# Kernel optimization log

Measured on AMD Instinct MI355X. Metric: run time of the kernel, lower is better.

The kernel has to match this reference:

```python
import jax, jax.numpy as jnp
import numpy as np

B, C, H, W = 2, 64, 64, 64
N = H * W

def _leaky(x):
    return jnp.where(x > 0, x, 0.1 * x)

def _conv1x1(x, w, b):
    # x: (B,C,H,W), w: (O,C), b: (O,)
    return jnp.einsum('bchw,oc->bohw', x, w) + b[None, :, None, None]

def _conv3x3(x, w, b=None):
    y = jax.lax.conv_general_dilated(x, w, (1, 1), 'SAME',
                                     dimension_numbers=('NCHW', 'OIHW', 'NCHW'))
    if b is not None:
        y = y + b[None, :, None, None]
    return y

def _add_coords(x):
    b, c, h, w = x.shape
    xx = (jnp.arange(w, dtype=x.dtype) / (w - 1)) * 2 - 1  # varies along width (last axis)
    yy = (jnp.arange(h, dtype=x.dtype) / (h - 1)) * 2 - 1  # varies along height
    xx = jnp.broadcast_to(xx[None, None, None, :], (b, 1, h, w))
    yy = jnp.broadcast_to(yy[None, None, :, None], (b, 1, h, w))
    return jnp.concatenate([x, xx, yy], axis=1)

def _channel_attn(x, lw, lb):
    # AdaptiveAvgPool2d(1) -> Linear(1,1) -> LeakyReLU(0.1) -> same Linear(1,1) -> Sigmoid
    p = x.mean(axis=(2, 3), keepdims=True)  # (B,C,1,1)
    h = _leaky(p * lw + lb)
    return jax.nn.sigmoid(h * lw + lb)

def _gated(x, lw, lb, coord_w):
    return _channel_attn(x, lw, lb) * _conv3x3(_add_coords(x), coord_w)

def reference(x, guide, lin_w, lin_b, coord_w,
              xq_w, xq_b, xk_w, xk_b, xv_w, xv_b,
              gq_w, gq_b, gk_w, gk_b,
              gamma, alpha, c1_w, c1_b, c2_w, c2_b, sc_w, sc_b):
    b, c, h, w = x.shape
    n = h * w
    xg = _gated(x, lin_w, lin_b, coord_w)       # (B,C,H,W)
    gg = _gated(guide, lin_w, lin_b, coord_w)

    xq = _conv1x1(xg, xq_w, xq_b).reshape(b, c, n)
    xk = _conv1x1(xg, xk_w, xk_b).reshape(b, c, n)
    xv = _conv1x1(xg, xv_w, xv_b).reshape(b, c, n)
    x_attn = jax.nn.softmax(jnp.einsum('bcn,bcm->bnm', xq, xk), axis=-1)  # (B,N,N)
    x_out = jnp.einsum('bcm,bnm->bcn', xv, x_attn).reshape(b, c, h, w)

    gq = _conv1x1(gg, gq_w, gq_b).reshape(b, c, n)
    gk = _conv1x1(gg, gk_w, gk_b).reshape(b, c, n)
    g_attn = jax.nn.softmax(jnp.einsum('bcn,bcm->bnm', gq, gk), axis=-1)  # (B,N,N)
    # guide_out deliberately uses x_value (as in the original forward)
    guide_out = jnp.einsum('bcm,bnm->bcn', xv, g_attn).reshape(b, c, h, w)

    out = gamma * x_out + alpha * guide_out
    branch = _conv3x3(_leaky(_conv3x3(_leaky(out), c1_w, c1_b)), c2_w, c2_b)
    return branch + _conv1x1(out, sc_w, sc_b) * guide_out

def setup_inputs() -> dict:
    key = jax.random.key(0)
    ks = jax.random.split(key, 32)
    f32 = jnp.float32
    def w1(k, o, i):
        return jax.random.normal(k, (o, i), f32) / np.sqrt(i).astype(np.float32)
    def w3(k, o, i):
        return jax.random.normal(k, (o, i, 3, 3), f32) / np.sqrt(i * 9).astype(np.float32)
    def bv(k, o):
        return jax.random.normal(k, (o,), f32) * 0.01
    return {
        'x': jax.random.normal(ks[0], (B, C, H, W), f32),
        'guide': jax.random.normal(ks[1], (B, C, H, W), f32),
        'lin_w': jax.random.normal(ks[2], (), f32),
        'lin_b': jax.random.normal(ks[3], (), f32) * 0.01,
        'coord_w': w3(ks[4], C, C + 2),
        'xq_w': w1(ks[5], C, C), 'xq_b': bv(ks[6], C),
        'xk_w': w1(ks[7], C, C), 'xk_b': bv(ks[8], C),
        'xv_w': w1(ks[9], C, C), 'xv_b': bv(ks[10], C),
        'gq_w': w1(ks[11], C, C), 'gq_b': bv(ks[12], C),
        'gk_w': w1(ks[13], C, C), 'gk_b': bv(ks[14], C),
        'gamma': jax.random.normal(ks[15], (1,), f32) * 0.5,
        'alpha': jax.random.normal(ks[16], (1,), f32) * 0.5,
        'c1_w': w3(ks[17], C, C), 'c1_b': bv(ks[18], C),
        'c2_w': w3(ks[19], C, C), 'c2_b': bv(ks[20], C),
        'sc_w': w1(ks[21], C, C), 'sc_b': bv(ks[22], C),
    }
```

## Files before the change

### kernel.cpp

```cpp
#include <hip/hip_runtime.h>
#include <hip/hip_bf16.h>

using bf16 = __hip_bfloat16;

#define DI __device__ __forceinline__

typedef __attribute__((ext_vector_type(8))) short short8;
typedef __attribute__((ext_vector_type(8))) unsigned short u16x8;
typedef __attribute__((ext_vector_type(4))) unsigned short u16x4;
typedef __attribute__((ext_vector_type(4))) float f32x4;

#define MFMA_BF16 __builtin_amdgcn_mfma_f32_16x16x32_bf16

DI float leaky(float x) { return x > 0.f ? x : 0.1f * x; }

DI unsigned short b16(float x) {
  union { float f; unsigned u; } v; v.f = x;
  unsigned r = v.u + 0x7FFFu + ((v.u >> 16) & 1u);
  return (unsigned short)(r >> 16);
}
DI float fromb16(unsigned short h) {
  union { unsigned u; float f; } v; v.u = ((unsigned)h) << 16; return v.f;
}

static constexpr int N_ = 4096;
static constexpr size_t CN = 262144;
static constexpr size_t BCN = 524288;

static constexpr size_t XG_OFF = 137104;
static constexpr size_t GG_OFF = XG_OFF + BCN;
static constexpr size_t QX_OFF = GG_OFF + BCN;
static constexpr size_t KX_OFF = QX_OFF + BCN;
static constexpr size_t VX_OFF = KX_OFF + BCN;
static constexpr size_t QG_OFF = VX_OFF + BCN;
static constexpr size_t KG_OFF = QG_OFF + BCN;
static constexpr size_t P1X_OFF = KG_OFF + BCN;
static constexpr size_t P1G_OFF = P1X_OFF + BCN;
static constexpr size_t ML_OFF  = P1G_OFF + BCN;
static constexpr size_t MLL_OFF = ML_OFF + 32768;
static constexpr size_t CA_OFF = ML_OFF;
static constexpr size_t OB_OFF = QX_OFF;
static constexpr size_t UB_OFF = KX_OFF;
static constexpr size_t GO_OFF = GG_OFF;
static constexpr size_t QXH_U = QX_OFF * 2, QXL_U = QXH_U + BCN;
static constexpr size_t KXH_U = KX_OFF * 2, KXL_U = KXH_U + BCN;
static constexpr size_t VXH_U = VX_OFF * 2;
static constexpr size_t QGH_U = QG_OFF * 2, QGL_U = QGH_U + BCN;
static constexpr size_t KGH_U = KG_OFF * 2, KGL_U = KGH_U + BCN;

__global__ __launch_bounds__(64) void k_ca(const float* __restrict__ x,
                                           const float* __restrict__ g,
                                           const float* __restrict__ lw_p,
                                           const float* __restrict__ lb_p,
                                           float* __restrict__ ws) {
  int blk = blockIdx.x;
  int ch = blk & 63; blk >>= 6;
  int b  = blk & 1;  blk >>= 1;
  int src = blk;
  const float* in = (src ? g : x) + ((size_t)(b * 64 + ch)) * N_;
  int t = threadIdx.x;
  float s = 0.f;
#pragma unroll
  for (int i = 0; i < 16; ++i) {
    float4 v = *reinterpret_cast<const float4*>(in + i * 256 + t * 4);
    s += (v.x + v.y) + (v.z + v.w);
  }
#pragma unroll
  for (int d = 1; d < 64; d <<= 1) s += __shfl_xor(s, d, 64);
  if (t == 0) {
    float p = s * (1.f / 4096.f);
    float lwv = lw_p[0], lbv = lb_p[0];
    float h = leaky(lwv * p + lbv);
    ws[CA_OFF + (src * 2 + b) * 64 + ch] = 1.f / (1.f + expf(-(lwv * h + lbv)));
  }
}

__global__ __launch_bounds__(256) void k_coordconv(const float* __restrict__ x,
                                                   const float* __restrict__ g,
                                                   const float* __restrict__ cw,
                                                   float* __restrict__ ws) {
  int blk = blockIdx.x;
  int row = blk & 63; blk >>= 6;
  int og  = blk & 15; blk >>= 4;
  int b   = blk & 1;  blk >>= 1;
  int src = blk;
  int o0 = og * 4;
  const float* in = src ? g : x;
  float* outp = ws + (src ? GG_OFF : XG_OFF);
  __shared__ __align__(16) float4 wl4[594];
  __shared__ float part[4][4][64];
  int t = threadIdx.x;
  int wv = t >> 6, px = t & 63;
  {
    float* wlf = (float*)wl4;
    for (int idx = t; idx < 2376; idx += 256)
      wlf[idx] = cw[(size_t)(o0 + (idx & 3)) * 594 + (idx >> 2)];
  }
  int rm = row - 1, rp = row + 1;
  int rmc = rm < 0 ? 0 : rm, rpc = rp > 63 ? 63 : rp;
  float maskm = rm < 0 ? 0.f : 1.f, maskp = rp > 63 ? 0.f : 1.f;
  int c0 = wv * 16;
  const float* base = in + ((size_t)(b * 64 + c0)) * N_ + px;
  float ra[16], rb[16], rc[16];
#pragma unroll
  for (int i = 0; i < 16; ++i) {
    ra[i] = base[(size_t)i * N_ + (size_t)rmc * 64] * maskm;
    rb[i] = base[(size_t)i * N_ + (size_t)row * 64];
    rc[i] = base[(size_t)i * N_ + (size_t)rpc * 64] * maskp;
  }
  float acc[4] = {};
  auto tap9 = [&](int ch, float va, float vb, float vc) {
    float la = __shfl_up(va, 1, 64);   if (px == 0)  la = 0.f;
    float ga = __shfl_down(va, 1, 64); if (px == 63) ga = 0.f;
    float lb = __shfl_up(vb, 1, 64);   if (px == 0)  lb = 0.f;
    float gb = __shfl_down(vb, 1, 64); if (px == 63) gb = 0.f;
    float lc = __shfl_up(vc, 1, 64);   if (px == 0)  lc = 0.f;
    float gc = __shfl_down(vc, 1, 64); if (px == 63) gc = 0.f;
    float4 w0 = wl4[ch * 9 + 0], w1 = wl4[ch * 9 + 1], w2 = wl4[ch * 9 + 2];
    float4 w3 = wl4[ch * 9 + 3], w4 = wl4[ch * 9 + 4], w5 = wl4[ch * 9 + 5];
    float4 w6 = wl4[ch * 9 + 6], w7 = wl4[ch * 9 + 7], w8 = wl4[ch * 9 + 8];
    acc[0] = fmaf(w0.x, la, fmaf(w1.x, va, fmaf(w2.x, ga, acc[0])));
    acc[1] = fmaf(w0.y, la, fmaf(w1.y, va, fmaf(w2.y, ga, acc[1])));
    acc[2] = fmaf(w0.z, la, fmaf(w1.z, va, fmaf(w2.z, ga, acc[2])));
    acc[3] = fmaf(w0.w, la, fmaf(w1.w, va, fmaf(w2.w, ga, acc[3])));
    acc[0] = fmaf(w3.x, lb, fmaf(w4.x, vb, fmaf(w5.x, gb, acc[0])));
    acc[1] = fmaf(w3.y, lb, fmaf(w4.y, vb, fmaf(w5.y, gb, acc[1])));
    acc[2] = fmaf(w3.z, lb, fmaf(w4.z, vb, fmaf(w5.z, gb, acc[2])));
    acc[3] = fmaf(w3.w, lb, fmaf(w4.w, vb, fmaf(w5.w, gb, acc[3])));
    acc[0] = fmaf(w6.x, lc, fmaf(w7.x, vc, fmaf(w8.x, gc, acc[0])));
    acc[1] = fmaf(w6.y, lc, fmaf(w7.y, vc, fmaf(w8.y, gc, acc[1])));
    acc[2] = fmaf(w6.z, lc, fmaf(w7.z, vc, fmaf(w8.z, gc, acc[2])));
    acc[3] = fmaf(w6.w, lc, fmaf(w7.w, vc, fmaf(w8.w, gc, acc[3])));
  };
  __syncthreads();
#pragma unroll
  for (int i = 0; i < 16; ++i) tap9(c0 + i, ra[i], rb[i], rc[i]);
  if (wv == 3) {
    float xx = (float)px * (2.f / 63.f) - 1.f;
    tap9(64, maskm * xx, xx, maskp * xx);
    float ya = maskm * ((float)rm * (2.f / 63.f) - 1.f);
    float yb = (float)row * (2.f / 63.f) - 1.f;
    float yc = maskp * ((float)rp * (2.f / 63.f) - 1.f);
    tap9(65, ya, yb, yc);
  }
#pragma unroll
  for (int oo = 0; oo < 4; ++oo) part[wv][oo][px] = acc[oo];
  __syncthreads();
  int oc = t >> 6;
  float s = (part[0][oc][px] + part[1][oc][px]) + (part[2][oc][px] + part[3][oc][px]);
  float cav = ws[CA_OFF + (src * 2 + b) * 64 + o0 + oc];
  outp[((size_t)(b * 64 + o0 + oc)) * N_ + (size_t)row * 64 + px] = s * cav;
}

__global__ __launch_bounds__(256) void k_proj(float* __restrict__ ws,
                                              const float* __restrict__ xqw, const float* __restrict__ xqb,
                                              const float* __restrict__ xkw, const float* __restrict__ xkb,
                                              const float* __restrict__ xvw, const float* __restrict__ xvb,
                                              const float* __restrict__ gqw, const float* __restrict__ gqb,
                                              const float* __restrict__ gkw, const float* __restrict__ gkb) {
  int blk = blockIdx.x;
  int pt = blk & 63; blk >>= 6;
  int b  = blk & 1;  blk >>= 1;
  int which = blk;
  size_t in_o;
  const float *wp, *bp;
  size_t hU = 0, lU = 0;
  if (which == 0)      { in_o = XG_OFF; wp = xqw; bp = xqb; hU = QXH_U; lU = QXL_U; }
  else if (which == 1) { in_o = XG_OFF; wp = xkw; bp = xkb; hU = KXH_U; lU = KXL_U; }
  else if (which == 2) { in_o = XG_OFF; wp = xvw; bp = xvb; }
  else if (which == 3) { in_o = GG_OFF; wp = gqw; bp = gqb; hU = QGH_U; lU = QGL_U; }
  else                 { in_o = GG_OFF; wp = gkw; bp = gkb; hU = KGH_U; lU = KGL_U; }

  __shared__ float tile[64 * 64];
  __shared__ float wl[64 * 65];
  __shared__ float bl[64];
  unsigned short* us = (unsigned short*)ws;
  int t = threadIdx.x;
  int pb = pt * 64;
  const float* in0 = ws + in_o + (size_t)b * CN + pb;
  for (int c0 = (t >> 6); c0 < 64; c0 += 4)
    tile[c0 * 64 + (t & 63)] = in0[(size_t)c0 * N_ + (t & 63)];
  for (int idx = t; idx < 4096; idx += 256)
    wl[(idx >> 6) * 65 + (idx & 63)] = wp[idx];
  if (t < 64) bl[t] = bp[t];
  __syncthreads();
  int o = t & 63, grp = t >> 6;
  const float* wr = &wl[o * 65];
  float acc[16];
  float bv = bl[o];
#pragma unroll
  for (int j = 0; j < 16; ++j) acc[j] = bv;
  for (int c = 0; c < 64; ++c) {
    float wv = wr[c];
    const float4* tb = reinterpret_cast<const float4*>(&tile[c * 64 + grp * 16]);
    float4 t0 = tb[0], t1 = tb[1], t2 = tb[2], t3 = tb[3];
    acc[0] = fmaf(wv, t0.x, acc[0]);   acc[1] = fmaf(wv, t0.y, acc[1]);
    acc[2] = fmaf(wv, t0.z, acc[2]);   acc[3] = fmaf(wv, t0.w, acc[3]);
    acc[4] = fmaf(wv, t1.x, acc[4]);   acc[5] = fmaf(wv, t1.y, acc[5]);
    acc[6] = fmaf(wv, t1.z, acc[6]);   acc[7] = fmaf(wv, t1.w, acc[7]);
    acc[8] = fmaf(wv, t2.x, acc[8]);   acc[9] = fmaf(wv, t2.y, acc[9]);
    acc[10] = fmaf(wv, t2.z, acc[10]); acc[11] = fmaf(wv, t2.w, acc[11]);
    acc[12] = fmaf(wv, t3.x, acc[12]); acc[13] = fmaf(wv, t3.y, acc[13]);
    acc[14] = fmaf(wv, t3.z, acc[14]); acc[15] = fmaf(wv, t3.w, acc[15]);
  }
  if (which != 2) {
#pragma unroll
    for (int j = 0; j < 16; ++j) {
      size_t idx = ((size_t)b * N_ + pb + grp * 16 + j) * 64 + o;
      unsigned short hi = b16(acc[j]);
      us[hU + idx] = hi;
      us[lU + idx] = b16(acc[j] - fromb16(hi));
    }
  } else {
    __syncthreads();
    float* ot = wl;
#pragma unroll
    for (int j = 0; j < 16; ++j) ot[o * 65 + grp * 16 + j] = acc[j];
    __syncthreads();
    int o2 = t >> 2;
#pragma unroll
    for (int e = 0; e < 4; ++e) {
      int px = (t & 3) * 16 + e * 4;
      u16x4 hv;
#pragma unroll
      for (int q = 0; q < 4; ++q) hv[q] = b16(ot[o2 * 65 + px + q]);
      size_t idx = ((size_t)(b * 64 + o2)) * N_ + pb + px;
      *reinterpret_cast<u16x4*>(&us[VXH_U + idx]) = hv;
    }
  }
}

__global__ __launch_bounds__(256) void k_attn(float* __restrict__ ws) {
  unsigned short* us = (unsigned short*)ws;
  int blk = blockIdx.x;
  int half = blk & 1; blk >>= 1;
  int qt = blk & 63;  blk >>= 6;
  int b  = blk & 1;   blk >>= 1;
  int at = blk;
  const unsigned short* QH = us + (at ? QGH_U : QXH_U);
  const unsigned short* QL = us + (at ? QGL_U : QXL_U);
  const unsigned short* KHg = us + (at ? KGH_U : KXH_U);
  const unsigned short* KLg = us + (at ? KGL_U : KXL_U);
  const unsigned short* VHg = us + VXH_U;
  float* Pg = ws + (at ? (half ? P1G_OFF : GG_OFF) : (half ? P1X_OFF : XG_OFF))
            + (size_t)b * CN + qt * 64;

  __shared__ unsigned short Kh[2][4096], Kl[2][4096], Vth[2][4096], Ph[4096];

  int t = threadIdx.x;
  int w = t >> 6, lane = t & 63, quad = lane >> 4, l15 = lane & 15;
  int swz = l15 & 7;

  short8 qh[2], ql[2];
  {
    size_t qbase = ((size_t)b * N_ + qt * 64 + 16 * w + l15) * 64;
#pragma unroll
    for (int ks = 0; ks < 2; ++ks) {
      qh[ks] = *reinterpret_cast<const short8*>(&QH[qbase + ks * 32 + quad * 8]);
      ql[ks] = *reinterpret_cast<const short8*>(&QL[qbase + ks * 32 + quad * 8]);
    }
  }

  short8 ones;
#pragma unroll
  for (int j = 0; j < 8; ++j) ones[j] = (short)0x3F80;

  int mt0 = half * 32, mt1 = half * 32 + 32;

  u16x8 rkh[2], rkl[2], rvh[2];
  size_t ko = ((size_t)b * N_ + (size_t)mt0 * 64 + (t >> 3)) * 64 + (size_t)(t & 7) * 8;
  size_t vo = ((size_t)(b * 64) + (t >> 3)) * N_ + (size_t)mt0 * 64 + (size_t)(t & 7) * 8;
  auto prefetch = [&]() {
    rkh[0] = *reinterpret_cast<const u16x8*>(&KHg[ko]);
    rkl[0] = *reinterpret_cast<const u16x8*>(&KLg[ko]);
    rkh[1] = *reinterpret_cast<const u16x8*>(&KHg[ko + 2048]);
    rkl[1] = *reinterpret_cast<const u16x8*>(&KLg[ko + 2048]);
    rvh[0] = *reinterpret_cast<const u16x8*>(&VHg[vo]);
    rvh[1] = *reinterpret_cast<const u16x8*>(&VHg[vo + (size_t)32 * N_]);
    ko += 4096; vo += 64;
  };
  int wr0 = t >> 3, wch = t & 7;
  int woff = wr0 * 64 + ((wch ^ (wr0 & 7)) << 3);
  auto writebuf = [&](int par) {
    *reinterpret_cast<u16x8*>(&Kh[par][woff]) = rkh[0];
    *reinterpret_cast<u16x8*>(&Kl[par][woff]) = rkl[0];
    *reinterpret_cast<u16x8*>(&Vth[par][woff]) = rvh[0];
    *reinterpret_cast<u16x8*>(&Kh[par][woff + 2048]) = rkh[1];
    *reinterpret_cast<u16x8*>(&Kl[par][woff + 2048]) = rkl[1];
    *reinterpret_cast<u16x8*>(&Vth[par][woff + 2048]) = rvh[1];
  };

  f32x4 Oa[4] = {{0.f, 0.f, 0.f, 0.f}, {0.f, 0.f, 0.f, 0.f},
                 {0.f, 0.f, 0.f, 0.f}, {0.f, 0.f, 0.f, 0.f}};
  f32x4 La = {0.f, 0.f, 0.f, 0.f};
  float M = -1e30f;

  int phb = (16 * w + l15) * 64;
  int mh = quad >> 1, mlw = (quad & 1) * 4;

  prefetch();
  writebuf(0);
  __syncthreads();
  for (int mt = mt0; mt < mt1; ++mt) {
    int pb = (mt - mt0) & 1;
    if (mt + 1 < mt1) prefetch();

    f32x4 S[4];
    __builtin_amdgcn_s_setprio(1);
#pragma unroll
    for (int ms = 0; ms < 4; ++ms) {
      f32x4 a0 = {0.f, 0.f, 0.f, 0.f}, a1 = {0.f, 0.f, 0.f, 0.f};
      int row = ms * 16 + l15;
#pragma unroll
      for (int ks = 0; ks < 2; ++ks) {
        int off = row * 64 + (((ks * 4 + quad) ^ swz) << 3);
        short8 khf = *reinterpret_cast<const short8*>(&Kh[pb][off]);
        short8 klf = *reinterpret_cast<const short8*>(&Kl[pb][off]);
        f32x4& a = ks ? a1 : a0;
        a = MFMA_BF16(khf, ql[ks], a, 0, 0, 0);
        a = MFMA_BF16(klf, qh[ks], a, 0, 0, 0);
        a = MFMA_BF16(khf, qh[ks], a, 0, 0, 0);
      }
      S[ms] = a0 + a1;
    }
    __builtin_amdgcn_s_setprio(0);

    float m0 = fmaxf(fmaxf(S[0][0], S[0][1]), fmaxf(S[0][2], S[0][3]));
    float m1 = fmaxf(fmaxf(S[1][0], S[1][1]), fmaxf(S[1][2], S[1][3]));
    float m2 = fmaxf(fmaxf(S[2][0], S[2][1]), fmaxf(S[2][2], S[2][3]));
    float m3 = fmaxf(fmaxf(S[3][0], S[3][1]), fmaxf(S[3][2], S[3][3]));
    float tm = fmaxf(fmaxf(m0, m1), fmaxf(m2, m3));
    tm = fmaxf(tm, __shfl_xor(tm, 16, 64));
    tm = fmaxf(tm, __shfl_xor(tm, 32, 64));
    float mn = fmaxf(M, tm);
    float al = __expf(M - mn);
    M = mn;
#pragma unroll
    for (int ms = 0; ms < 4; ++ms) {
      int goff = phb + ((((ms << 1) + mh) ^ swz) << 3) + mlw;
#pragma unroll
      for (int r = 0; r < 4; ++r) {
        float p = __expf(S[ms][r] - mn);
        Ph[goff + r] = b16(p);
      }
    }
#pragma unroll
    for (int cs = 0; cs < 4; ++cs) {
      Oa[cs][0] *= al; Oa[cs][1] *= al; Oa[cs][2] *= al; Oa[cs][3] *= al;
    }
    La[0] *= al;

    __builtin_amdgcn_s_setprio(1);
#pragma unroll
    for (int ks = 0; ks < 2; ++ks) {
      int poff = phb + (((ks * 4 + quad) ^ swz) << 3);
      short8 phf = *reinterpret_cast<const short8*>(&Ph[poff]);
      La = MFMA_BF16(ones, phf, La, 0, 0, 0);
#pragma unroll
      for (int cs = 0; cs < 4; ++cs) {
        int voff = (cs * 16 + l15) * 64 + (((ks * 4 + quad) ^ swz) << 3);
        short8 vhf = *reinterpret_cast<const short8*>(&Vth[pb][voff]);
        Oa[cs] = MFMA_BF16(vhf, phf, Oa[cs], 0, 0, 0);
      }
    }
    __builtin_amdgcn_s_setprio(0);

    if (mt + 1 < mt1) writebuf(pb ^ 1);
    __syncthreads();
  }

#pragma unroll
  for (int cs = 0; cs < 4; ++cs) {
#pragma unroll
    for (int r = 0; r < 4; ++r) {
      int c = cs * 16 + quad * 4 + r;
      Pg[(size_t)c * N_ + 16 * w + l15] = Oa[cs][r];
    }
  }
  if (quad == 0) {
    int mlb = ((at * 2 + half) * 2 + b) * 4096 + qt * 64 + 16 * w + l15;
    ws[ML_OFF + mlb] = M;
    ws[MLL_OFF + mlb] = La[0];
  }
}

__global__ __launch_bounds__(256) void k_merge(float* __restrict__ ws,
                                               const float* __restrict__ gm_p,
                                               const float* __restrict__ al_p) {
  size_t i4 = (size_t)blockIdx.x * 256 + threadIdx.x;
  size_t i = i4 * 4;
  int n = (int)(i & 4095);
  int b = (int)(i >> 18);
  float gm = gm_p[0], al = al_p[0];
  float4 p0x = *reinterpret_cast<const float4*>(ws + XG_OFF + i);
  float4 p1x = *reinterpret_cast<const float4*>(ws + P1X_OFF + i);
  float4 p0g = *reinterpret_cast<const float4*>(ws + GG_OFF + i);
  float4 p1g = *reinterpret_cast<const float4*>(ws + P1G_OFF + i);
  float4 M0x = *reinterpret_cast<const float4*>(ws + ML_OFF  + (0 + b) * 4096 + n);
  float4 L0x = *reinterpret_cast<const float4*>(ws + MLL_OFF + (0 + b) * 4096 + n);
  float4 M1x = *reinterpret_cast<const float4*>(ws + ML_OFF  + (2 + b) * 4096 + n);
  float4 L1x = *reinterpret_cast<const float4*>(ws + MLL_OFF + (2 + b) * 4096 + n);
  float4 M0g = *reinterpret_cast<const float4*>(ws + ML_OFF  + (4 + b) * 4096 + n);
  float4 L0g = *reinterpret_cast<const float4*>(ws + MLL_OFF + (4 + b) * 4096 + n);
  float4 M1g = *reinterpret_cast<const float4*>(ws + ML_OFF  + (6 + b) * 4096 + n);
  float4 L1g = *reinterpret_cast<const float4*>(ws + MLL_OFF + (6 + b) * 4096 + n);
  const float* p0xv = (const float*)&p0x; const float* p1xv = (const float*)&p1x;
  const float* p0gv = (const float*)&p0g; const float* p1gv = (const float*)&p1g;
  const float* m0xv = (const float*)&M0x; const float* l0xv = (const float*)&L0x;
  const float* m1xv = (const float*)&M1x; const float* l1xv = (const float*)&L1x;
  const float* m0gv = (const float*)&M0g; const float* l0gv = (const float*)&L0g;
  const float* m1gv = (const float*)&M1g; const float* l1gv = (const float*)&L1g;
  float4 go, ob;
  float* gov = (float*)&go; float* obv = (float*)&ob;
#pragma unroll
  for (int l = 0; l < 4; ++l) {
    float mx = fmaxf(m0xv[l], m1xv[l]);
    float w0 = __expf(m0xv[l] - mx), w1 = __expf(m1xv[l] - mx);
    float xc = (p0xv[l] * w0 + p1xv[l] * w1) / (l0xv[l] * w0 + l1xv[l] * w1);
    float mg = fmaxf(m0gv[l], m1gv[l]);
    float v0 = __expf(m0gv[l] - mg), v1 = __expf(m1gv[l] - mg);
    float gc = (p0gv[l] * v0 + p1gv[l] * v1) / (l0gv[l] * v0 + l1gv[l] * v1);
    gov[l] = gc;
    obv[l] = gm * xc + al * gc;
  }
  *reinterpret_cast<float4*>(ws + GG_OFF + i) = go;
  *reinterpret_cast<float4*>(ws + QX_OFF + i) = ob;
}

__global__ __launch_bounds__(256) void k_conv1(float* __restrict__ ws,
                                               const float* __restrict__ c1w,
                                               const float* __restrict__ c1b) {
  int blk = blockIdx.x;
  int row = blk & 63; blk >>= 6;
  int og  = blk & 15; blk >>= 4;
  int b   = blk;
  int o0 = og * 4;
  __shared__ __align__(16) float4 wl4[576];
  __shared__ float part[4][4][64];
  int t = threadIdx.x;
  int wv = t >> 6, px = t & 63;
  {
    float* wlf = (float*)wl4;
    for (int idx = t; idx < 2304; idx += 256)
      wlf[idx] = c1w[(size_t)(o0 + (idx & 3)) * 576 + (idx >> 2)];
  }
  int rm = row - 1, rp = row + 1;
  int rmc = rm < 0 ? 0 : rm, rpc = rp > 63 ? 63 : rp;
  float maskm = rm < 0 ? 0.f : 1.f, maskp = rp > 63 ? 0.f : 1.f;
  int c0 = wv * 16;
  const float* base = ws + OB_OFF + (size_t)b * CN + (size_t)c0 * N_ + px;
  float ra[16], rb[16], rc[16];
#pragma unroll
  for (int i = 0; i < 16; ++i) {
    ra[i] = leaky(base[(size_t)i * N_ + (size_t)rmc * 64]) * maskm;
    rb[i] = leaky(base[(size_t)i * N_ + (size_t)row * 64]);
    rc[i] = leaky(base[(size_t)i * N_ + (size_t)rpc * 64]) * maskp;
  }
  float acc[4] = {};
  auto tap9 = [&](int ch, float va, float vb, float vc) {
    float la = __shfl_up(va, 1, 64);   if (px == 0)  la = 0.f;
    float ga = __shfl_down(va, 1, 64); if (px == 63) ga = 0.f;
    float lb = __shfl_up(vb, 1, 64);   if (px == 0)  lb = 0.f;
    float gb = __shfl_down(vb, 1, 64); if (px == 63) gb = 0.f;
    float lc = __shfl_up(vc, 1, 64);   if (px == 0)  lc = 0.f;
    float gc = __shfl_down(vc, 1, 64); if (px == 63) gc = 0.f;
    float4 w0 = wl4[ch * 9 + 0], w1 = wl4[ch * 9 + 1], w2 = wl4[ch * 9 + 2];
    float4 w3 = wl4[ch * 9 + 3], w4 = wl4[ch * 9 + 4], w5 = wl4[ch * 9 + 5];
    float4 w6 = wl4[ch * 9 + 6], w7 = wl4[ch * 9 + 7], w8 = wl4[ch * 9 + 8];
    acc[0] = fmaf(w0.x, la, fmaf(w1.x, va, fmaf(w2.x, ga, acc[0])));
    acc[1] = fmaf(w0.y, la, fmaf(w1.y, va, fmaf(w2.y, ga, acc[1])));
    acc[2] = fmaf(w0.z, la, fmaf(w1.z, va, fmaf(w2.z, ga, acc[2])));
    acc[3] = fmaf(w0.w, la, fmaf(w1.w, va, fmaf(w2.w, ga, acc[3])));
    acc[0] = fmaf(w3.x, lb, fmaf(w4.x, vb, fmaf(w5.x, gb, acc[0])));
    acc[1] = fmaf(w3.y, lb, fmaf(w4.y, vb, fmaf(w5.y, gb, acc[1])));
    acc[2] = fmaf(w3.z, lb, fmaf(w4.z, vb, fmaf(w5.z, gb, acc[2])));
    acc[3] = fmaf(w3.w, lb, fmaf(w4.w, vb, fmaf(w5.w, gb, acc[3])));
    acc[0] = fmaf(w6.x, lc, fmaf(w7.x, vc, fmaf(w8.x, gc, acc[0])));
    acc[1] = fmaf(w6.y, lc, fmaf(w7.y, vc, fmaf(w8.y, gc, acc[1])));
    acc[2] = fmaf(w6.z, lc, fmaf(w7.z, vc, fmaf(w8.z, gc, acc[2])));
    acc[3] = fmaf(w6.w, lc, fmaf(w7.w, vc, fmaf(w8.w, gc, acc[3])));
  };
  __syncthreads();
#pragma unroll
  for (int i = 0; i < 16; ++i) tap9(c0 + i, ra[i], rb[i], rc[i]);
#pragma unroll
  for (int oo = 0; oo < 4; ++oo) part[wv][oo][px] = acc[oo];
  __syncthreads();
  int oc = t >> 6;
  float s = (part[0][oc][px] + part[1][oc][px]) + (part[2][oc][px] + part[3][oc][px]);
  float* ub = ws + UB_OFF + (size_t)b * CN;
  ub[(size_t)(o0 + oc) * N_ + (size_t)row * 64 + px] = leaky(s + c1b[o0 + oc]);
}

__global__ __launch_bounds__(256) void k_final(const float* __restrict__ ws,
                                               const float* __restrict__ c2w,
                                               const float* __restrict__ c2b,
                                               const float* __restrict__ scw,
                                               const float* __restrict__ scb,
                                               float* __restrict__ out) {
  int blk = blockIdx.x;
  int row = blk & 63; blk >>= 6;
  int og  = blk & 15; blk >>= 4;
  int b   = blk;
  int o0 = og * 4;
  __shared__ __align__(16) float4 wl4[576];
  __shared__ __align__(16) float4 scl4[64];
  __shared__ float part[4][4][64];
  __shared__ float part2[4][4][64];
  int t = threadIdx.x;
  int wv = t >> 6, px = t & 63;
  {
    float* wlf = (float*)wl4;
    for (int idx = t; idx < 2304; idx += 256)
      wlf[idx] = c2w[(size_t)(o0 + (idx & 3)) * 576 + (idx >> 2)];
    float* sclf = (float*)scl4;
    if (t < 256) {
      int idx = t;
      sclf[idx] = scw[(size_t)(o0 + (idx & 3)) * 64 + (idx >> 2)];
    }
  }
  int rm = row - 1, rp = row + 1;
  int rmc = rm < 0 ? 0 : rm, rpc = rp > 63 ? 63 : rp;
  float maskm = rm < 0 ? 0.f : 1.f, maskp = rp > 63 ? 0.f : 1.f;
  int c0 = wv * 16;
  const float* base = ws + UB_OFF + (size_t)b * CN + (size_t)c0 * N_ + px;
  const float* obb  = ws + OB_OFF + (size_t)b * CN + (size_t)c0 * N_ + (size_t)row * 64 + px;
  float ra[16], rb[16], rc[16], ob[16];
#pragma unroll
  for (int i = 0; i < 16; ++i) {
    ra[i] = base[(size_t)i * N_ + (size_t)rmc * 64] * maskm;
    rb[i] = base[(size_t)i * N_ + (size_t)row * 64];
    rc[i] = base[(size_t)i * N_ + (size_t)rpc * 64] * maskp;
    ob[i] = obb[(size_t)i * N_];
  }
  float acc[4] = {};
  float scp[4] = {};
  auto tap9 = [&](int ch, float va, float vb, float vc) {
    float la = __shfl_up(va, 1, 64);   if (px == 0)  la = 0.f;
    float ga = __shfl_down(va, 1, 64); if (px == 63) ga = 0.f;
    float lb = __shfl_up(vb, 1, 64);   if (px == 0)  lb = 0.f;
    float gb = __shfl_down(vb, 1, 64); if (px == 63) gb = 0.f;
    float lc = __shfl_up(vc, 1, 64);   if (px == 0)  lc = 0.f;
    float gc = __shfl_down(vc, 1, 64); if (px == 63) gc = 0.f;
    float4 w0 = wl4[ch * 9 + 0], w1 = wl4[ch * 9 + 1], w2 = wl4[ch * 9 + 2];
    float4 w3 = wl4[ch * 9 + 3], w4 = wl4[ch * 9 + 4], w5 = wl4[ch * 9 + 5];
    float4 w6 = wl4[ch * 9 + 6], w7 = wl4[ch * 9 + 7], w8 = wl4[ch * 9 + 8];
    acc[0] = fmaf(w0.x, la, fmaf(w1.x, va, fmaf(w2.x, ga, acc[0])));
    acc[1] = fmaf(w0.y, la, fmaf(w1.y, va, fmaf(w2.y, ga, acc[1])));
    acc[2] = fmaf(w0.z, la, fmaf(w1.z, va, fmaf(w2.z, ga, acc[2])));
    acc[3] = fmaf(w0.w, la, fmaf(w1.w, va, fmaf(w2.w, ga, acc[3])));
    acc[0] = fmaf(w3.x, lb, fmaf(w4.x, vb, fmaf(w5.x, gb, acc[0])));
    acc[1] = fmaf(w3.y, lb, fmaf(w4.y, vb, fmaf(w5.y, gb, acc[1])));
    acc[2] = fmaf(w3.z, lb, fmaf(w4.z, vb, fmaf(w5.z, gb, acc[2])));
    acc[3] = fmaf(w3.w, lb, fmaf(w4.w, vb, fmaf(w5.w, gb, acc[3])));
    acc[0] = fmaf(w6.x, lc, fmaf(w7.x, vc, fmaf(w8.x, gc, acc[0])));
    acc[1] = fmaf(w6.y, lc, fmaf(w7.y, vc, fmaf(w8.y, gc, acc[1])));
    acc[2] = fmaf(w6.z, lc, fmaf(w7.z, vc, fmaf(w8.z, gc, acc[2])));
    acc[3] = fmaf(w6.w, lc, fmaf(w7.w, vc, fmaf(w8.w, gc, acc[3])));
  };
  __syncthreads();
#pragma unroll
  for (int i = 0; i < 16; ++i) {
    tap9(c0 + i, ra[i], rb[i], rc[i]);
    float4 s4 = scl4[c0 + i];
    scp[0] = fmaf(s4.x, ob[i], scp[0]);
    scp[1] = fmaf(s4.y, ob[i], scp[1]);
    scp[2] = fmaf(s4.z, ob[i], scp[2]);
    scp[3] = fmaf(s4.w, ob[i], scp[3]);
  }
#pragma unroll
  for (int oo = 0; oo < 4; ++oo) {
    part[wv][oo][px] = acc[oo];
    part2[wv][oo][px] = scp[oo];
  }
  __syncthreads();
  int oc = t >> 6;
  float s  = (part[0][oc][px] + part[1][oc][px]) + (part[2][oc][px] + part[3][oc][px]);
  float sc = (part2[0][oc][px] + part2[1][oc][px]) + (part2[2][oc][px] + part2[3][oc][px]);
  const float* go = ws + GO_OFF + (size_t)b * CN;
  size_t pix = (size_t)row * 64 + px;
  float gvv = go[(size_t)(o0 + oc) * N_ + pix];
  out[(size_t)b * CN + (size_t)(o0 + oc) * N_ + pix] =
      (s + c2b[o0 + oc]) + (sc + scb[o0 + oc]) * gvv;
}

extern "C" void kernel_launch(void* const* d_in, const int* in_sizes, int n_in,
                              void* d_out, int out_size, void* d_ws, size_t ws_size,
                              hipStream_t stream) {
  const float* x     = (const float*)d_in[0];
  const float* guide = (const float*)d_in[1];
  const float* lin_w = (const float*)d_in[2];
  const float* lin_b = (const float*)d_in[3];
  const float* cw    = (const float*)d_in[4];
  const float* xq_w  = (const float*)d_in[5];
  const float* xq_b  = (const float*)d_in[6];
  const float* xk_w  = (const float*)d_in[7];
  const float* xk_b  = (const float*)d_in[8];
  const float* xv_w  = (const float*)d_in[9];
  const float* xv_b  = (const float*)d_in[10];
  const float* gq_w  = (const float*)d_in[11];
  const float* gq_b  = (const float*)d_in[12];
  const float* gk_w  = (const float*)d_in[13];
  const float* gk_b  = (const float*)d_in[14];
  const float* gamma = (const float*)d_in[15];
  const float* alpha = (const float*)d_in[16];
  const float* c1_w  = (const float*)d_in[17];
  const float* c1_b  = (const float*)d_in[18];
  const float* c2_w  = (const float*)d_in[19];
  const float* c2_b  = (const float*)d_in[20];
  const float* sc_w  = (const float*)d_in[21];
  const float* sc_b  = (const float*)d_in[22];
  float* out = (float*)d_out;
  float* ws = (float*)d_ws;

  k_ca<<<256, 64, 0, stream>>>(x, guide, lin_w, lin_b, ws);
  k_coordconv<<<4096, 256, 0, stream>>>(x, guide, cw, ws);
  k_proj<<<640, 256, 0, stream>>>(ws, xq_w, xq_b, xk_w, xk_b, xv_w, xv_b,
                                  gq_w, gq_b, gk_w, gk_b);
  k_attn<<<512, 256, 0, stream>>>(ws);
  k_merge<<<512, 256, 0, stream>>>(ws, gamma, alpha);
  k_conv1<<<2048, 256, 0, stream>>>(ws, c1_w, c1_b);
  k_final<<<2048, 256, 0, stream>>>(ws, c2_w, c2_b, sc_w, sc_b, out);
}
```

Measured before the change: 269.9 us.

## Split attention KV range across two thread groups and load V directly to registers

Each attention block now runs 512 threads as two 256-thread groups. Each group processes half of the key tiles with its own double-buffered K staging, and the two partial softmax states (max, sum, output) are merged in LDS at the end. V fragments are loaded straight from global memory into registers instead of being staged through LDS, and P values are written to LDS as packed 64-bit stores. This doubles parallelism per query tile and shortens the serial loop, at the cost of higher register and LDS pressure, uncoalesced-looking V loads, and an extra merge step.

```diff
diff --git a/kernel.cpp b/kernel.cpp
--- a/kernel.cpp
+++ b/kernel.cpp
@@ -230,7 +230,7 @@
   }
 }
 
-__global__ __launch_bounds__(256) void k_attn(float* __restrict__ ws) {
+__global__ __launch_bounds__(512, 4) void k_attn(float* __restrict__ ws) {
   unsigned short* us = (unsigned short*)ws;
   int blk = blockIdx.x;
   int half = blk & 1; blk >>= 1;
@@ -245,11 +245,15 @@
   float* Pg = ws + (at ? (half ? P1G_OFF : GG_OFF) : (half ? P1X_OFF : XG_OFF))
             + (size_t)b * CN + qt * 64;
 
-  __shared__ unsigned short Kh[2][4096], Kl[2][4096], Vth[2][4096], Ph[4096];
+  __shared__ __align__(16) unsigned short lds[40960];
 
   int t = threadIdx.x;
-  int w = t >> 6, lane = t & 63, quad = lane >> 4, l15 = lane & 15;
+  int g = t >> 8, tg = t & 255;
+  int w = tg >> 6, lane = tg & 63, quad = lane >> 4, l15 = lane & 15;
   int swz = l15 & 7;
+  unsigned short* Kh0 = lds + g * 20480;
+  unsigned short* Kl0 = lds + g * 20480 + 8192;
+  unsigned short* Phg = lds + g * 20480 + 16384;
 
   short8 qh[2], ql[2];
   {
@@ -265,30 +269,27 @@
 #pragma unroll
   for (int j = 0; j < 8; ++j) ones[j] = (short)0x3F80;
 
-  int mt0 = half * 32, mt1 = half * 32 + 32;
-
-  u16x8 rkh[2], rkl[2], rvh[2];
-  size_t ko = ((size_t)b * N_ + (size_t)mt0 * 64 + (t >> 3)) * 64 + (size_t)(t & 7) * 8;
-  size_t vo = ((size_t)(b * 64) + (t >> 3)) * N_ + (size_t)mt0 * 64 + (size_t)(t & 7) * 8;
-  auto prefetch = [&]() {
+  int mt0 = half * 32 + g * 16;
+
+  u16x8 rkh[2], rkl[2];
+  size_t ko = ((size_t)b * N_ + (size_t)mt0 * 64 + (tg >> 3)) * 64 + (size_t)(tg & 7) * 8;
+  auto prefetchK = [&]() {
     rkh[0] = *reinterpret_cast<const u16x8*>(&KHg[ko]);
     rkl[0] = *reinterpret_cast<const u16x8*>(&KLg[ko]);
     rkh[1] = *reinterpret_cast<const u16x8*>(&KHg[ko + 2048]);
     rkl[1] = *reinterpret_cast<const u16x8*>(&KLg[ko + 2048]);
-    rvh[0] = *reinterpret_cast<const u16x8*>(&VHg[vo]);
-    rvh[1] = *reinterpret_cast<const u16x8*>(&VHg[vo + (size_t)32 * N_]);
-    ko += 4096; vo += 64;
+    ko += 4096;
   };
-  int wr0 = t >> 3, wch = t & 7;
+  int wr0 = tg >> 3, wch = tg & 7;
   int woff = wr0 * 64 + ((wch ^ (wr0 & 7)) << 3);
-  auto writebuf = [&](int par) {
-    *reinterpret_cast<u16x8*>(&Kh[par][woff]) = rkh[0];
-    *reinterpret_cast<u16x8*>(&Kl[par][woff]) = rkl[0];
-    *reinterpret_cast<u16x8*>(&Vth[par][woff]) = rvh[0];
-    *reinterpret_cast<u16x8*>(&Kh[par][woff + 2048]) = rkh[1];
-    *reinterpret_cast<u16x8*>(&Kl[par][woff + 2048]) = rkl[1];
-    *reinterpret_cast<u16x8*>(&Vth[par][woff + 2048]) = rvh[1];
+  auto writebufK = [&](int par) {
+    *reinterpret_cast<u16x8*>(&Kh0[par * 4096 + woff]) = rkh[0];
+    *reinterpret_cast<u16x8*>(&Kl0[par * 4096 + woff]) = rkl[0];
+    *reinterpret_cast<u16x8*>(&Kh0[par * 4096 + woff + 2048]) = rkh[1];
+    *reinterpret_cast<u16x8*>(&Kl0[par * 4096 + woff + 2048]) = rkl[1];
   };
+
+  size_t vb = ((size_t)(b * 64 + l15)) * N_ + (size_t)mt0 * 64 + quad * 8;
 
   f32x4 Oa[4] = {{0.f, 0.f, 0.f, 0.f}, {0.f, 0.f, 0.f, 0.f},
                  {0.f, 0.f, 0.f, 0.f}, {0.f, 0.f, 0.f, 0.f}};
@@ -298,12 +299,19 @@
   int phb = (16 * w + l15) * 64;
   int mh = quad >> 1, mlw = (quad & 1) * 4;
 
-  prefetch();
-  writebuf(0);
-  __syncthreads();
-  for (int mt = mt0; mt < mt1; ++mt) {
-    int pb = (mt - mt0) & 1;
-    if (mt + 1 < mt1) prefetch();
+  prefetchK();
+  writebufK(0);
+  __syncthreads();
+  for (int it = 0; it < 16; ++it) {
+    int pb = it & 1;
+    u16x8 rv[8];
+#pragma unroll
+    for (int cs = 0; cs < 4; ++cs)
+#pragma unroll
+      for (int ks = 0; ks < 2; ++ks)
+        rv[cs * 2 + ks] = *reinterpret_cast<const u16x8*>(&VHg[vb + (size_t)cs * 16 * N_ + ks * 32]);
+    vb += 64;
+    if (it + 1 < 16) prefetchK();
 
     f32x4 S[4];
     __builtin_amdgcn_s_setprio(1);
@@ -313,9 +321,9 @@
       int row = ms * 16 + l15;
 #pragma unroll
       for (int ks = 0; ks < 2; ++ks) {
-        int off = row * 64 + (((ks * 4 + quad) ^ swz) << 3);
-        short8 khf = *reinterpret_cast<const short8*>(&Kh[pb][off]);
-        short8 klf = *reinterpret_cast<const short8*>(&Kl[pb][off]);
+        int off = pb * 4096 + row * 64 + (((ks * 4 + quad) ^ swz) << 3);
+        short8 khf = *reinterpret_cast<const short8*>(&Kh0[off]);
+        short8 klf = *reinterpret_cast<const short8*>(&Kl0[off]);
         f32x4& a = ks ? a1 : a0;
         a = MFMA_BF16(khf, ql[ks], a, 0, 0, 0);
         a = MFMA_BF16(klf, qh[ks], a, 0, 0, 0);
@@ -325,11 +333,14 @@
     }
     __builtin_amdgcn_s_setprio(0);
 
-    float m0 = fmaxf(fmaxf(S[0][0], S[0][1]), fmaxf(S[0][2], S[0][3]));
-    float m1 = fmaxf(fmaxf(S[1][0], S[1][1]), fmaxf(S[1][2], S[1][3]));
-    float m2 = fmaxf(fmaxf(S[2][0], S[2][1]), fmaxf(S[2][2], S[2][3]));
-    float m3 = fmaxf(fmaxf(S[3][0], S[3][1]), fmaxf(S[3][2], S[3][3]));
-    float tm = fmaxf(fmaxf(m0, m1), fmaxf(m2, m3));
+    float t0 = fmaxf(fmaxf(S[0][0], S[0][1]), S[0][2]);
+    float t1 = fmaxf(fmaxf(S[0][3], S[1][0]), S[1][1]);
+    float t2 = fmaxf(fmaxf(S[1][2], S[1][3]), S[2][0]);
+    float t3 = fmaxf(fmaxf(S[2][1], S[2][2]), S[2][3]);
+    float t4 = fmaxf(fmaxf(S[3][0], S[3][1]), S[3][2]);
+    float t5 = fmaxf(fmaxf(t0, t1), t2);
+    float t6 = fmaxf(fmaxf(t3, t4), S[3][3]);
+    float tm = fmaxf(t5, t6);
     tm = fmaxf(tm, __shfl_xor(tm, 16, 64));
     tm = fmaxf(tm, __shfl_xor(tm, 32, 64));
     float mn = fmaxf(M, tm);
@@ -338,11 +349,12 @@
 #pragma unroll
     for (int ms = 0; ms < 4; ++ms) {
       int goff = phb + ((((ms << 1) + mh) ^ swz) << 3) + mlw;
-#pragma unroll
-      for (int r = 0; r < 4; ++r) {
-        float p = __expf(S[ms][r] - mn);
-        Ph[goff + r] = b16(p);
-      }
+      unsigned lo = (unsigned)b16(__expf(S[ms][0] - mn)) |
+                    ((unsigned)b16(__expf(S[ms][1] - mn)) << 16);
+      unsigned hi = (unsigned)b16(__expf(S[ms][2] - mn)) |
+                    ((unsigned)b16(__expf(S[ms][3] - mn)) << 16);
+      uint2 pk; pk.x = lo; pk.y = hi;
+      *reinterpret_cast<uint2*>(&Phg[goff]) = pk;
     }
 #pragma unroll
     for (int cs = 0; cs < 4; ++cs) {
@@ -354,33 +366,53 @@
 #pragma unroll
     for (int ks = 0; ks < 2; ++ks) {
       int poff = phb + (((ks * 4 + quad) ^ swz) << 3);
-      short8 phf = *reinterpret_cast<const short8*>(&Ph[poff]);
+      short8 phf = *reinterpret_cast<const short8*>(&Phg[poff]);
       La = MFMA_BF16(ones, phf, La, 0, 0, 0);
 #pragma unroll
       for (int cs = 0; cs < 4; ++cs) {
-        int voff = (cs * 16 + l15) * 64 + (((ks * 4 + quad) ^ swz) << 3);
-        short8 vhf = *reinterpret_cast<const short8*>(&Vth[pb][voff]);
+        short8 vhf = (short8)rv[cs * 2 + ks];
         Oa[cs] = MFMA_BF16(vhf, phf, Oa[cs], 0, 0, 0);
       }
     }
     __builtin_amdgcn_s_setprio(0);
 
-    if (mt + 1 < mt1) writebuf(pb ^ 1);
+    if (it + 1 < 16) writebufK(pb ^ 1);
     __syncthreads();
   }
 
-#pragma unroll
-  for (int cs = 0; cs < 4; ++cs) {
-#pragma unroll
-    for (int r = 0; r < 4; ++r) {
-      int c = cs * 16 + quad * 4 + r;
-      Pg[(size_t)c * N_ + 16 * w + l15] = Oa[cs][r];
-    }
-  }
-  if (quad == 0) {
-    int mlb = ((at * 2 + half) * 2 + b) * 4096 + qt * 64 + 16 * w + l15;
-    ws[ML_OFF + mlb] = M;
-    ws[MLL_OFF + mlb] = La[0];
+  float* exch = (float*)(lds + 20480);
+  float Lv = La[0];
+  if (g == 1) {
+#pragma unroll
+    for (int cs = 0; cs < 4; ++cs)
+#pragma unroll
+      for (int r = 0; r < 4; ++r) exch[tg * 16 + cs * 4 + r] = Oa[cs][r];
+    if (quad == 0) {
+      exch[4096 + 16 * w + l15] = M;
+      exch[4160 + 16 * w + l15] = Lv;
+    }
+  }
+  __syncthreads();
+  if (g == 0) {
+    int n = 16 * w + l15;
+    float MB = exch[4096 + n], LB = exch[4160 + n];
+    float Mm = fmaxf(M, MB);
+    float wA = __expf(M - Mm), wB = __expf(MB - Mm);
+    float Lm = Lv * wA + LB * wB;
+#pragma unroll
+    for (int cs = 0; cs < 4; ++cs) {
+#pragma unroll
+      for (int r = 0; r < 4; ++r) {
+        float o = Oa[cs][r] * wA + exch[tg * 16 + cs * 4 + r] * wB;
+        int c = cs * 16 + quad * 4 + r;
+        Pg[(size_t)c * N_ + n] = o;
+      }
+    }
+    if (quad == 0) {
+      int mlb = ((at * 2 + half) * 2 + b) * 4096 + qt * 64 + n;
+      ws[ML_OFF + mlb] = Mm;
+      ws[MLL_OFF + mlb] = Lm;
+    }
   }
 }
 
@@ -617,7 +649,7 @@
   k_coordconv<<<4096, 256, 0, stream>>>(x, guide, cw, ws);
   k_proj<<<640, 256, 0, stream>>>(ws, xq_w, xq_b, xk_w, xk_b, xv_w, xv_b,
                                   gq_w, gq_b, gk_w, gk_b);
-  k_attn<<<512, 256, 0, stream>>>(ws);
+  k_attn<<<512, 512, 0, stream>>>(ws);
   k_merge<<<512, 256, 0, stream>>>(ws, gamma, alpha);
   k_conv1<<<2048, 256, 0, stream>>>(ws, c1_w, c1_b);
   k_final<<<2048, 256, 0, stream>>>(ws, c2_w, c2_b, sc_w, sc_b, out);
```

Measured after the change: 308.1 us. 14.2% more time.

## Load V fragments directly from global into registers, bypassing LDS staging

Applied to the files above, without the earlier changes.

Drops the shared-memory double buffer for V. Each wave now loads its V MFMA operands straight from global memory into registers, split into two halves issued before and after the QK^T MFMAs so the loads can overlap compute. This removes LDS writes, LDS reads and a third of the shared footprint, which may raise occupancy, but every wave now fetches V separately from global/L2 with 16-byte strided loads. The change also packs the four bf16 P values into one 8-byte LDS store and rebalances the max-reduction tree.

```diff
diff --git a/kernel.cpp b/kernel.cpp
--- a/kernel.cpp
+++ b/kernel.cpp
@@ -245,7 +245,7 @@
   float* Pg = ws + (at ? (half ? P1G_OFF : GG_OFF) : (half ? P1X_OFF : XG_OFF))
             + (size_t)b * CN + qt * 64;
 
-  __shared__ unsigned short Kh[2][4096], Kl[2][4096], Vth[2][4096], Ph[4096];
+  __shared__ unsigned short Kh[2][4096], Kl[2][4096], Ph[4096];
 
   int t = threadIdx.x;
   int w = t >> 6, lane = t & 63, quad = lane >> 4, l15 = lane & 15;
@@ -267,28 +267,25 @@
 
   int mt0 = half * 32, mt1 = half * 32 + 32;
 
-  u16x8 rkh[2], rkl[2], rvh[2];
+  u16x8 rkh[2], rkl[2];
   size_t ko = ((size_t)b * N_ + (size_t)mt0 * 64 + (t >> 3)) * 64 + (size_t)(t & 7) * 8;
-  size_t vo = ((size_t)(b * 64) + (t >> 3)) * N_ + (size_t)mt0 * 64 + (size_t)(t & 7) * 8;
-  auto prefetch = [&]() {
+  auto prefetchK = [&]() {
     rkh[0] = *reinterpret_cast<const u16x8*>(&KHg[ko]);
     rkl[0] = *reinterpret_cast<const u16x8*>(&KLg[ko]);
     rkh[1] = *reinterpret_cast<const u16x8*>(&KHg[ko + 2048]);
     rkl[1] = *reinterpret_cast<const u16x8*>(&KLg[ko + 2048]);
-    rvh[0] = *reinterpret_cast<const u16x8*>(&VHg[vo]);
-    rvh[1] = *reinterpret_cast<const u16x8*>(&VHg[vo + (size_t)32 * N_]);
-    ko += 4096; vo += 64;
+    ko += 4096;
   };
   int wr0 = t >> 3, wch = t & 7;
   int woff = wr0 * 64 + ((wch ^ (wr0 & 7)) << 3);
-  auto writebuf = [&](int par) {
+  auto writebufK = [&](int par) {
     *reinterpret_cast<u16x8*>(&Kh[par][woff]) = rkh[0];
     *reinterpret_cast<u16x8*>(&Kl[par][woff]) = rkl[0];
-    *reinterpret_cast<u16x8*>(&Vth[par][woff]) = rvh[0];
     *reinterpret_cast<u16x8*>(&Kh[par][woff + 2048]) = rkh[1];
     *reinterpret_cast<u16x8*>(&Kl[par][woff + 2048]) = rkl[1];
-    *reinterpret_cast<u16x8*>(&Vth[par][woff + 2048]) = rvh[1];
   };
+
+  size_t vb = ((size_t)(b * 64 + l15)) * N_ + (size_t)mt0 * 64 + quad * 8;
 
   f32x4 Oa[4] = {{0.f, 0.f, 0.f, 0.f}, {0.f, 0.f, 0.f, 0.f},
                  {0.f, 0.f, 0.f, 0.f}, {0.f, 0.f, 0.f, 0.f}};
@@ -298,12 +295,16 @@
   int phb = (16 * w + l15) * 64;
   int mh = quad >> 1, mlw = (quad & 1) * 4;
 
-  prefetch();
-  writebuf(0);
+  prefetchK();
+  writebufK(0);
   __syncthreads();
   for (int mt = mt0; mt < mt1; ++mt) {
     int pb = (mt - mt0) & 1;
-    if (mt + 1 < mt1) prefetch();
+    u16x8 rvA[4];
+#pragma unroll
+    for (int cs = 0; cs < 4; ++cs)
+      rvA[cs] = *reinterpret_cast<const u16x8*>(&VHg[vb + (size_t)cs * 16 * N_]);
+    if (mt + 1 < mt1) prefetchK();
 
     f32x4 S[4];
     __builtin_amdgcn_s_setprio(1);
@@ -325,11 +326,20 @@
     }
     __builtin_amdgcn_s_setprio(0);
 
-    float m0 = fmaxf(fmaxf(S[0][0], S[0][1]), fmaxf(S[0][2], S[0][3]));
-    float m1 = fmaxf(fmaxf(S[1][0], S[1][1]), fmaxf(S[1][2], S[1][3]));
-    float m2 = fmaxf(fmaxf(S[2][0], S[2][1]), fmaxf(S[2][2], S[2][3]));
-    float m3 = fmaxf(fmaxf(S[3][0], S[3][1]), fmaxf(S[3][2], S[3][3]));
-    float tm = fmaxf(fmaxf(m0, m1), fmaxf(m2, m3));
+    u16x8 rvB[4];
+#pragma unroll
+    for (int cs = 0; cs < 4; ++cs)
+      rvB[cs] = *reinterpret_cast<const u16x8*>(&VHg[vb + (size_t)cs * 16 * N_ + 32]);
+    vb += 64;
+
+    float t0 = fmaxf(fmaxf(S[0][0], S[0][1]), S[0][2]);
+    float t1 = fmaxf(fmaxf(S[0][3], S[1][0]), S[1][1]);
+    float t2 = fmaxf(fmaxf(S[1][2], S[1][3]), S[2][0]);
+    float t3 = fmaxf(fmaxf(S[2][1], S[2][2]), S[2][3]);
+    float t4 = fmaxf(fmaxf(S[3][0], S[3][1]), S[3][2]);
+    float t5 = fmaxf(fmaxf(t0, t1), t2);
+    float t6 = fmaxf(fmaxf(t3, t4), S[3][3]);
+    float tm = fmaxf(t5, t6);
     tm = fmaxf(tm, __shfl_xor(tm, 16, 64));
     tm = fmaxf(tm, __shfl_xor(tm, 32, 64));
     float mn = fmaxf(M, tm);
@@ -338,11 +348,12 @@
 #pragma unroll
     for (int ms = 0; ms < 4; ++ms) {
       int goff = phb + ((((ms << 1) + mh) ^ swz) << 3) + mlw;
-#pragma unroll
-      for (int r = 0; r < 4; ++r) {
-        float p = __expf(S[ms][r] - mn);
-        Ph[goff + r] = b16(p);
-      }
+      unsigned lo = (unsigned)b16(__expf(S[ms][0] - mn)) |
+                    ((unsigned)b16(__expf(S[ms][1] - mn)) << 16);
+      unsigned hi = (unsigned)b16(__expf(S[ms][2] - mn)) |
+                    ((unsigned)b16(__expf(S[ms][3] - mn)) << 16);
+      uint2 pk; pk.x = lo; pk.y = hi;
+      *reinterpret_cast<uint2*>(&Ph[goff]) = pk;
     }
 #pragma unroll
     for (int cs = 0; cs < 4; ++cs) {
@@ -351,21 +362,25 @@
     La[0] *= al;
 
     __builtin_amdgcn_s_setprio(1);
-#pragma unroll
-    for (int ks = 0; ks < 2; ++ks) {
-      int poff = phb + (((ks * 4 + quad) ^ swz) << 3);
+    {
+      int poff = phb + ((quad ^ swz) << 3);
       short8 phf = *reinterpret_cast<const short8*>(&Ph[poff]);
       La = MFMA_BF16(ones, phf, La, 0, 0, 0);
 #pragma unroll
-      for (int cs = 0; cs < 4; ++cs) {
-        int voff = (cs * 16 + l15) * 64 + (((ks * 4 + quad) ^ swz) << 3);
-        short8 vhf = *reinterpret_cast<const short8*>(&Vth[pb][voff]);
-        Oa[cs] = MFMA_BF16(vhf, phf, Oa[cs], 0, 0, 0);
-      }
+      for (int cs = 0; cs < 4; ++cs)
+        Oa[cs] = MFMA_BF16((short8)rvA[cs], phf, Oa[cs], 0, 0, 0);
+    }
+    {
+      int poff = phb + (((4 + quad) ^ swz) << 3);
+      short8 phf = *reinterpret_cast<const short8*>(&Ph[poff]);
+      La = MFMA_BF16(ones, phf, La, 0, 0, 0);
+#pragma unroll
+      for (int cs = 0; cs < 4; ++cs)
+        Oa[cs] = MFMA_BF16((short8)rvB[cs], phf, Oa[cs], 0, 0, 0);
     }
     __builtin_amdgcn_s_setprio(0);
 
-    if (mt + 1 < mt1) writebuf(pb ^ 1);
+    if (mt + 1 < mt1) writebufK(pb ^ 1);
     __syncthreads();
   }
 
```

New measurement: 277.1 us. +2.7%, slower.
